# Kernel tuning notes

Hardware: AMD Instinct MI355X
Metric: run time of the kernel (lower is better)

Reference implementation:

```python
import jax, jax.numpy as jnp
import numpy as np

KH, KW, PAD, DIL, STRIDE = 3, 3, 1, 1, 1


def _conv2d(x, w):
    # plain dense conv, NCHW / OIHW, stride 1, pad 1
    return jax.lax.conv_general_dilated(
        x, w, window_strides=(STRIDE, STRIDE),
        padding=[(PAD, PAD), (PAD, PAD)],
        rhs_dilation=(DIL, DIL),
        dimension_numbers=('NCHW', 'OIHW', 'NCHW'))


def _deform_patches(x, offset):
    """Bilinear-sample deformable patches.
    x: [B,C,H,W], offset: [B,2K,Ho,Wo] with per-tap (dy,dx).
    Returns [B,C,K,Ho,Wo]."""
    B, C, H, W = x.shape
    Ho, Wo = offset.shape[2], offset.shape[3]
    K = KH * KW
    off = offset.reshape(B, K, 2, Ho, Wo)

    ky = jnp.repeat(jnp.arange(KH), KW)            # [K]
    kx = jnp.tile(jnp.arange(KW), KH)              # [K]
    base_y = (jnp.arange(Ho) * STRIDE - PAD)[None, :, None] + (DIL * ky)[:, None, None]  # [K,Ho,1]
    base_x = (jnp.arange(Wo) * STRIDE - PAD)[None, None, :] + (DIL * kx)[:, None, None]  # [K,1,Wo]

    sy = base_y[None].astype(x.dtype) + off[:, :, 0]   # [B,K,Ho,Wo]
    sx = base_x[None].astype(x.dtype) + off[:, :, 1]

    y0 = jnp.floor(sy); x0 = jnp.floor(sx)
    ly = sy - y0;       lx = sx - x0
    y0i = y0.astype(jnp.int32); x0i = x0.astype(jnp.int32)

    x_flat = x.reshape(B, C, H * W)

    def corner(yi, xi, wgt):
        valid = (yi >= 0) & (yi < H) & (xi >= 0) & (xi < W)   # zero padding outside
        idx = (jnp.clip(yi, 0, H - 1) * W + jnp.clip(xi, 0, W - 1))  # [B,K,Ho,Wo]
        gath = jax.vmap(lambda img, i: img[:, i.reshape(-1)])(x_flat, idx)  # [B,C,K*Ho*Wo]
        gath = gath.reshape(B, C, K, Ho, Wo)
        return gath * (wgt * valid.astype(x.dtype))[:, None]

    p = corner(y0i,     x0i,     (1 - ly) * (1 - lx))
    p = p + corner(y0i,     x0i + 1, (1 - ly) * lx)
    p = p + corner(y0i + 1, x0i,     ly * (1 - lx))
    p = p + corner(y0i + 1, x0i + 1, ly * lx)
    return p  # [B,C,K,Ho,Wo]


def setup_inputs() -> dict:
    key = jax.random.key(0)
    k1, k2, k3 = jax.random.split(key, 3)
    B, C, H, W = 8, 256, 64, 64
    Cout = 256
    x = jax.random.normal(k1, (B, C, H, W), dtype=jnp.float32)
    offset_w = jax.random.normal(k2, (2 * KH * KW, C, KH, KW), dtype=jnp.float32) * 0.02
    deform_w = jax.random.normal(k3, (Cout, C, KH, KW), dtype=jnp.float32) * 0.02
    return {"x": x, "offset_w": offset_w, "deform_w": deform_w}


def reference(x, offset_w, deform_w):
    # 1) offset-predicting conv
    offset = _conv2d(x, offset_w)                    # [B,2K,H,W]
    # 2) deformable conv = bilinear gather + contraction over (Cin, K)
    patches = _deform_patches(x, offset)             # [B,C,K,H,W]
    Cout = deform_w.shape[0]
    wk = deform_w.reshape(Cout, deform_w.shape[1], KH * KW)
    y = jnp.einsum('bckhw,ock->bohw', patches, wk)   # [B,Cout,H,W]
    # 3) avg + std channel attention (torch.std default: unbiased, ddof=1)
    avg = jnp.mean(y, axis=(2, 3), keepdims=True)
    std = jnp.std(y, axis=(2, 3), keepdims=True, ddof=1)
    attn = jax.nn.sigmoid(avg + std)
    return y * attn
```

## Files before the change

kernel.cpp:

```cpp
#include <hip/hip_runtime.h>
#include <hip/hip_bf16.h>
#include <math.h>

#define C_IN 256
#define H_   64
#define W_   64
#define B_   8
#define COUT 256
#define HW   (H_*W_)

typedef float f32x4 __attribute__((ext_vector_type(4)));
typedef float f32x2 __attribute__((ext_vector_type(2)));
typedef short short8 __attribute__((ext_vector_type(8)));

static __device__ __forceinline__ int pack_bf16x2(float a, float b) {
    __hip_bfloat162 h = __float22bfloat162_rn(make_float2(a, b));
    union { __hip_bfloat162 h; int i; } u; u.h = h;
    return u.i;
}

static __device__ __forceinline__ f32x2 up2(int v) {
    union { int i; float f; } a, b;
    a.i = v << 16;
    b.i = v & 0xffff0000;
    f32x2 r; r[0] = a.f; r[1] = b.f;
    return r;
}

__global__ __launch_bounds__(256) void prep_weights_kernel(
    const float* __restrict__ ow, const float* __restrict__ dw,
    short* __restrict__ wR, short* __restrict__ wO)
{
    int blk = blockIdx.x;
    int k   = blk / 288;
    int row = blk % 288;
    int c   = threadIdx.x;
    int cblk = c >> 6, ks = (c >> 5) & 1, q = (c >> 3) & 3, ce = c & 7;
    union { float f; unsigned u; } a;
    if (row < 256) {
        int o = row;
        a.f = dw[(size_t)o * 2304 + c * 9 + k];
        unsigned r = (a.u + 0x7fffu + ((a.u >> 16) & 1u)) >> 16;
        size_t idx = (size_t)(k * 8 + cblk * 2 + ks) * 8192
                   + (size_t)(o >> 4) * 512 + q * 128 + (o & 15) * 8 + ce;
        wR[idx] = (short)r;
    } else {
        int o = row - 256;
        a.f = (o < 18) ? ow[(size_t)o * 2304 + c * 9 + k] : 0.f;
        unsigned r = (a.u + 0x7fffu + ((a.u >> 16) & 1u)) >> 16;
        size_t idx = (size_t)(k * 8 + cblk * 2 + ks) * 1024
                   + (size_t)(o >> 4) * 512 + q * 128 + (o & 15) * 8 + ce;
        wO[idx] = (short)r;
    }
}

__global__ __launch_bounds__(256) void transpose_x_kernel(
    const float* __restrict__ x, unsigned short* __restrict__ xT)
{
    __shared__ float tile[64][257];
    const int tid = threadIdx.x;
    const int b = blockIdx.x >> 6, h = blockIdx.x & 63;
    const float* xb = x + ((size_t)b << 20) + h * 64;

#pragma unroll
    for (int pass = 0; pass < 16; ++pass) {
        int c  = pass * 16 + (tid >> 4);
        int w0 = (tid & 15) * 4;
        float4 v = *(const float4*)(xb + (size_t)c * 4096 + w0);
        tile[w0][c] = v.x; tile[w0 + 1][c] = v.y;
        tile[w0 + 2][c] = v.z; tile[w0 + 3][c] = v.w;
    }
    __syncthreads();

    int4* ob = (int4*)(xT + ((size_t)blockIdx.x << 14));
#pragma unroll
    for (int pass = 0; pass < 8; ++pass) {
        int idx = pass * 256 + tid;
        int w = idx >> 5, ch8 = idx & 31;
        const float* tr = &tile[w][ch8 * 8];
        int4 pk;
        pk.x = pack_bf16x2(tr[0], tr[1]);
        pk.y = pack_bf16x2(tr[2], tr[3]);
        pk.z = pack_bf16x2(tr[4], tr[5]);
        pk.w = pack_bf16x2(tr[6], tr[7]);
        ob[idx] = pk;
    }
}

__global__ __launch_bounds__(256, 2) void offset_mfma_kernel(
    const unsigned short* __restrict__ xT, const short* __restrict__ wO,
    float* __restrict__ offs)
{
    __shared__ int4 xtile[3 * 66 * 8];

    const int tid = threadIdx.x;
    const int b   = blockIdx.x & 7;
    const int ho  = blockIdx.x >> 3;

    const int wv = tid >> 6;
    const int ln = tid & 63;
    const int lo = ln & 15;
    const int quad = ln >> 4;

    f32x4 acc[2];
    acc[0] = (f32x4){0.f, 0.f, 0.f, 0.f};
    acc[1] = (f32x4){0.f, 0.f, 0.f, 0.f};

    const unsigned short* xbb = xT + ((size_t)b << 20);
    const int4 zero4 = {0, 0, 0, 0};

    const int srow = tid >> 6;
    const int spx  = tid & 63;
    const int syy  = ho + srow - 1;
    const bool svalid = (srow < 3) && (syy >= 0) && (syy < 64);
    const int syc  = min(max(syy, 0), 63);
    const unsigned short* sbase = xbb + (((size_t)(syc * 64 + spx)) << 8);
    const int sslot = spx + 1;

#define OLOAD(CH, G)                                                          \
    if (srow < 3) {                                                           \
        const int4* sp_ = (const int4*)(sbase + (CH));                        \
        _Pragma("unroll")                                                     \
        for (int j = 0; j < 8; ++j) G[j] = sp_[j];                            \
    }
#define OCOMMIT(G)                                                            \
    if (srow < 3) {                                                           \
        _Pragma("unroll")                                                     \
        for (int j = 0; j < 8; ++j)                                           \
            xtile[(srow * 66 + sslot) * 8 + (j ^ (sslot & 7))]                \
                = svalid ? G[j] : zero4;                                      \
    }

    auto mfmaC = [&](int chunk) {
        __builtin_amdgcn_s_setprio(1);
#pragma unroll
        for (int ky = 0; ky < 3; ++ky) {
#pragma unroll
            for (int kx = 0; kx < 3; ++kx) {
#pragma unroll
                for (int ks = 0; ks < 2; ++ks) {
                    int ps = wv * 16 + lo + kx;
                    int cslot = (ks * 4 + quad) ^ (ps & 7);
                    short8 bfr = *(const short8*)&xtile[(ky * 66 + ps) * 8 + cslot];
                    const short* wkb = wO
                        + (size_t)((ky * 3 + kx) * 8 + chunk * 2 + ks) * 1024
                        + ln * 8;
#pragma unroll
                    for (int t = 0; t < 2; ++t) {
                        short8 afr = *(const short8*)(wkb + t * 512);
                        acc[t] = __builtin_amdgcn_mfma_f32_16x16x32_bf16(
                            afr, bfr, acc[t], 0, 0, 0);
                    }
                }
            }
        }
        __builtin_amdgcn_s_setprio(0);
    };

    int4 ga[8], gb[8];
    OLOAD(0, ga);
    OCOMMIT(ga);
    if (srow == 3 && (tid & 63) < 6) {
        int idx = tid & 63;
        int row_ = idx >> 1, s_ = (idx & 1) * 65;
#pragma unroll
        for (int j = 0; j < 8; ++j) xtile[(row_ * 66 + s_) * 8 + j] = zero4;
    }
    __syncthreads();

    OLOAD(64, gb);
    __builtin_amdgcn_sched_barrier(0);
    mfmaC(0);
    __syncthreads();
    OCOMMIT(gb);
    __syncthreads();

    OLOAD(128, ga);
    __builtin_amdgcn_sched_barrier(0);
    mfmaC(1);
    __syncthreads();
    OCOMMIT(ga);
    __syncthreads();

    OLOAD(192, gb);
    __builtin_amdgcn_sched_barrier(0);
    mfmaC(2);
    __syncthreads();
    OCOMMIT(gb);
    __syncthreads();

    mfmaC(3);
#undef OLOAD
#undef OCOMMIT

#pragma unroll
    for (int t = 0; t < 2; ++t) {
#pragma unroll
        for (int r = 0; r < 4; ++r) {
            int o = t * 16 + quad * 4 + r;
            if (o < 18)
                offs[((size_t)b * 18 + o) * HW + ho * 64 + wv * 16 + lo] = acc[t][r];
        }
    }
}

struct afrag { short8 v[2][4]; };

__global__ __launch_bounds__(256, 2) void deform_mfma_kernel(
    const unsigned short* __restrict__ xT, const float* __restrict__ offs,
    const short* __restrict__ wR, float* __restrict__ y,
    float* __restrict__ sum_, float* __restrict__ sumsq_)
{
    __shared__ int4   meta_i[576];
    __shared__ float4 meta_w[576];
    __shared__ int4   bT[2][64 * 8];

    const int tid = threadIdx.x;
    const int b   = blockIdx.x & 7;
    const int ho  = blockIdx.x >> 3;

    for (int e = tid; e < 576; e += 256) {
        int kk  = e >> 6;
        int pxe = e & 63;
        float dy = offs[((size_t)b * 18 + 2 * kk)     * HW + ho * W_ + pxe];
        float dx = offs[((size_t)b * 18 + 2 * kk + 1) * HW + ho * W_ + pxe];
        float sy = (float)(ho - 1 + kk / 3) + dy;
        float sx = (float)(pxe - 1 + kk % 3) + dx;
        float y0f = floorf(sy), x0f = floorf(sx);
        float ly = sy - y0f, lx = sx - x0f;
        int y0 = (int)y0f, x0 = (int)x0f;
        int y1 = y0 + 1, x1 = x0 + 1;
        float wy0 = 1.f - ly, wx0 = 1.f - lx;
        bool vy0 = (y0 >= 0) & (y0 < H_), vy1 = (y1 >= 0) & (y1 < H_);
        bool vx0 = (x0 >= 0) & (x0 < W_), vx1 = (x1 >= 0) & (x1 < W_);
        int cy0 = min(max(y0, 0), H_ - 1), cy1 = min(max(y1, 0), H_ - 1);
        int cx0 = min(max(x0, 0), W_ - 1), cx1 = min(max(x1, 0), W_ - 1);
        int4 ii; float4 ww;
        ii.x = (cy0 * W_ + cx0) << 9;  ww.x = wy0 * wx0 * ((vy0 & vx0) ? 1.f : 0.f);
        ii.y = (cy0 * W_ + cx1) << 9;  ww.y = wy0 * lx  * ((vy0 & vx1) ? 1.f : 0.f);
        ii.z = (cy1 * W_ + cx0) << 9;  ww.z = ly  * wx0 * ((vy1 & vx0) ? 1.f : 0.f);
        ii.w = (cy1 * W_ + cx1) << 9;  ww.w = ly  * lx  * ((vy1 & vx1) ? 1.f : 0.f);
        meta_i[e] = ii;
        meta_w[e] = ww;
    }

    const int px = tid >> 2;
    const int cg = tid & 3;
    const int wv = tid >> 6;
    const int ln = tid & 63;
    const int lo = ln & 15;
    const int quad = ln >> 4;

    f32x4 acc[4][4];
#pragma unroll
    for (int t = 0; t < 4; ++t)
#pragma unroll
        for (int p = 0; p < 4; ++p)
            acc[t][p] = (f32x4){0.f, 0.f, 0.f, 0.f};

    const char* xbb = (const char*)(xT + ((size_t)b << 20) + cg * 16);

#define ISSUE_G(S, G0,G1,G2,G3,G4,G5,G6,G7)                                   \
    {                                                                         \
        int kn_ = (S) >> 2, cn_ = ((S) & 3) << 7;                             \
        int4 ii_ = meta_i[kn_ * 64 + px];                                     \
        const char* xc_ = xbb + cn_;                                          \
        const int4* pA_ = (const int4*)(xc_ + ii_.x);                         \
        const int4* pB_ = (const int4*)(xc_ + ii_.y);                         \
        const int4* pC_ = (const int4*)(xc_ + ii_.z);                         \
        const int4* pD_ = (const int4*)(xc_ + ii_.w);                         \
        G0 = pA_[0]; G1 = pA_[1];                                             \
        G2 = pB_[0]; G3 = pB_[1];                                             \
        G4 = pC_[0]; G5 = pC_[1];                                             \
        G6 = pD_[0]; G7 = pD_[1];                                             \
    }

#define ISSUE_A(S, AF)                                                        \
    {                                                                         \
        const short* wkb_ = wR + (size_t)((((S) >> 2) * 8 + ((S) & 3) * 2))   \
                          * 8192 + wv * 2048 + ln * 8;                        \
        _Pragma("unroll")                                                     \
        for (int ks_ = 0; ks_ < 2; ++ks_)                                     \
            _Pragma("unroll")                                                 \
            for (int t_ = 0; t_ < 4; ++t_)                                    \
                AF.v[ks_][t_] = *(const short8*)(wkb_ + ks_ * 8192 + t_ * 512);\
    }

#define BLEND_W(S, BUF, G0,G1,G2,G3,G4,G5,G6,G7)                              \
    {                                                                         \
        int kn_ = (S) >> 2;                                                   \
        float4 w4_ = meta_w[kn_ * 64 + px];                                   \
        auto bl_ = [&](int av, int bv, int cv, int dv) -> int {               \
            f32x2 r_ = up2(av) * w4_.x + up2(bv) * w4_.y                      \
                     + up2(cv) * w4_.z + up2(dv) * w4_.w;                     \
            return pack_bf16x2(r_[0], r_[1]);                                 \
        };                                                                    \
        int4 o0_, o1_;                                                        \
        o0_.x = bl_(G0.x, G2.x, G4.x, G6.x);                                  \
        o0_.y = bl_(G0.y, G2.y, G4.y, G6.y);                                  \
        o0_.z = bl_(G0.z, G2.z, G4.z, G6.z);                                  \
        o0_.w = bl_(G0.w, G2.w, G4.w, G6.w);                                  \
        o1_.x = bl_(G1.x, G3.x, G5.x, G7.x);                                  \
        o1_.y = bl_(G1.y, G3.y, G5.y, G7.y);                                  \
        o1_.z = bl_(G1.z, G3.z, G5.z, G7.z);                                  \
        o1_.w = bl_(G1.w, G3.w, G5.w, G7.w);                                  \
        bT[BUF][px * 8 + ((2 * cg)     ^ (px & 7))] = o0_;                    \
        bT[BUF][px * 8 + ((2 * cg + 1) ^ (px & 7))] = o1_;                    \
    }

    auto mfmaStage = [&](int buf, const afrag& AF) {
        __builtin_amdgcn_s_setprio(1);
#pragma unroll
        for (int ks = 0; ks < 2; ++ks) {
            int ch = ks * 4 + quad;
            short8 bfr[4];
#pragma unroll
            for (int p = 0; p < 4; ++p) {
                int pp = p * 16 + lo;
                bfr[p] = *(const short8*)&bT[buf][pp * 8 + (ch ^ (pp & 7))];
            }
#pragma unroll
            for (int t = 0; t < 4; ++t)
#pragma unroll
                for (int p = 0; p < 4; ++p)
                    acc[t][p] = __builtin_amdgcn_mfma_f32_16x16x32_bf16(
                        AF.v[ks][t], bfr[p], acc[t][p], 0, 0, 0);
        }
        __builtin_amdgcn_s_setprio(0);
    };

    int4 a0, a1, a2, a3, a4, a5, a6, a7;
    int4 b0, b1, b2, b3, b4, b5, b6, b7;
    afrag afrA, afrB;

    __syncthreads();

    ISSUE_A(0, afrA);
    ISSUE_G(0, a0,a1,a2,a3,a4,a5,a6,a7);
    ISSUE_G(1, b0,b1,b2,b3,b4,b5,b6,b7);
    BLEND_W(0, 0, a0,a1,a2,a3,a4,a5,a6,a7);
    __syncthreads();

#pragma unroll 1
    for (int t = 0; t < 17; ++t) {
        int s = 2 * t;
        ISSUE_A(s + 1, afrB);
        ISSUE_G(s + 2, a0,a1,a2,a3,a4,a5,a6,a7);
        __builtin_amdgcn_sched_barrier(0);
        mfmaStage(0, afrA);
        BLEND_W(s + 1, 1, b0,b1,b2,b3,b4,b5,b6,b7);
        __syncthreads();
        ISSUE_A(s + 2, afrA);
        ISSUE_G(s + 3, b0,b1,b2,b3,b4,b5,b6,b7);
        __builtin_amdgcn_sched_barrier(0);
        mfmaStage(1, afrB);
        BLEND_W(s + 2, 0, a0,a1,a2,a3,a4,a5,a6,a7);
        __syncthreads();
    }
    ISSUE_A(35, afrB);
    __builtin_amdgcn_sched_barrier(0);
    mfmaStage(0, afrA);
    BLEND_W(35, 1, b0,b1,b2,b3,b4,b5,b6,b7);
    __syncthreads();
    mfmaStage(1, afrB);

#undef ISSUE_G
#undef ISSUE_A
#undef BLEND_W

    float* yb = y + ((size_t)b << 20) + ho * 64;
#pragma unroll
    for (int t = 0; t < 4; ++t) {
#pragma unroll
        for (int r = 0; r < 4; ++r) {
            int o = wv * 64 + t * 16 + quad * 4 + r;
            float sv = 0.f, qv = 0.f;
#pragma unroll
            for (int p = 0; p < 4; ++p) {
                float val = acc[t][p][r];
                yb[(size_t)o * HW + p * 16 + lo] = val;
                sv += val;
                qv += val * val;
            }
#pragma unroll
            for (int m = 1; m <= 8; m <<= 1) {
                sv += __shfl_xor(sv, m, 16);
                qv += __shfl_xor(qv, m, 16);
            }
            if (lo == 0) {
                atomicAdd(&sum_[b * COUT + o], sv);
                atomicAdd(&sumsq_[b * COUT + o], qv);
            }
        }
    }
}

__global__ __launch_bounds__(256) void attn_scale_kernel(
    const float* __restrict__ sum_, const float* __restrict__ sumsq_,
    float* __restrict__ y)
{
    int bo = blockIdx.x;
    float s = sum_[bo], q = sumsq_[bo];
    float mean = s * (1.f / 4096.f);
    float var  = (q - s * s * (1.f / 4096.f)) * (1.f / 4095.f);
    float sd   = sqrtf(fmaxf(var, 0.f));
    float attn = 1.f / (1.f + expf(-(mean + sd)));
    float4* yp = (float4*)(y + (size_t)bo * HW);
#pragma unroll
    for (int i = 0; i < 4; ++i) {
        float4 v = yp[threadIdx.x + i * 256];
        v.x *= attn; v.y *= attn; v.z *= attn; v.w *= attn;
        yp[threadIdx.x + i * 256] = v;
    }
}

extern "C" void kernel_launch(void* const* d_in, const int* in_sizes, int n_in,
                              void* d_out, int out_size, void* d_ws, size_t ws_size,
                              hipStream_t stream)
{
    const float* x  = (const float*)d_in[0];
    const float* ow = (const float*)d_in[1];
    const float* dw = (const float*)d_in[2];
    float* out = (float*)d_out;
    float* ws  = (float*)d_ws;

    float*          offs = ws;
    unsigned short* xT   = (unsigned short*)(ws + 589824);
    short*          wR   = (short*)(xT + 8388608);
    short*          wO   = wR + 589824;
    float*          sum_ = (float*)(wO + 73728);
    float*          sumsq_ = sum_ + 2048;

    hipMemsetAsync(sum_, 0, 2 * 2048 * sizeof(float), stream);

    prep_weights_kernel<<<9 * 288, 256, 0, stream>>>(ow, dw, wR, wO);
    transpose_x_kernel<<<512, 256, 0, stream>>>(x, xT);
    offset_mfma_kernel<<<512, 256, 0, stream>>>(xT, wO, offs);
    deform_mfma_kernel<<<512, 256, 0, stream>>>(xT, offs, wR, out, sum_, sumsq_);
    attn_scale_kernel<<<2048, 256, 0, stream>>>(sum_, sumsq_, out);
}
```

Baseline: 199.2 us.

## Process two output rows per deform block with 512 threads and fp16 bilinear weights

The deformable conv kernel now handles two output rows (128 pixels) per block with 512 threads and 8 waves. Each wave computes 32 output channels across 8 pixel tiles instead of 64 channels across 4. Each weight fragment is now reused over twice as many pixels, which halves total weight traffic and the block count. The bilinear corner weights are stored in LDS as packed fp16 to keep LDS use down, at some cost in precision. Register pressure and occupancy shift because of the larger block and the different accumulator shape.

After: 200.2 us. About the same (+0.5%).

```diff
diff --git a/kernel.cpp b/kernel.cpp
--- a/kernel.cpp
+++ b/kernel.cpp
@@ -1,5 +1,6 @@
 #include <hip/hip_runtime.h>
 #include <hip/hip_bf16.h>
+#include <hip/hip_fp16.h>
 #include <math.h>
 
 #define C_IN 256
@@ -24,6 +25,18 @@
     a.i = v << 16;
     b.i = v & 0xffff0000;
     f32x2 r; r[0] = a.f; r[1] = b.f;
+    return r;
+}
+
+static __device__ __forceinline__ unsigned pkhalf2(float a, float b) {
+    __half2 h = __floats2half2_rn(a, b);
+    union { __half2 h; unsigned u; } c; c.h = h;
+    return c.u;
+}
+static __device__ __forceinline__ f32x2 uphalf2(unsigned v) {
+    union { unsigned u; __half2 h; } c; c.u = v;
+    float2 f = __half22float2(c.h);
+    f32x2 r; r[0] = f.x; r[1] = f.y;
     return r;
 }
 
@@ -204,28 +217,31 @@
     }
 }
 
-struct afrag { short8 v[2][4]; };
-
-__global__ __launch_bounds__(256, 2) void deform_mfma_kernel(
+struct afrag2 { short8 v[2][2]; };
+
+__global__ __launch_bounds__(512, 2) void deform_mfma_kernel(
     const unsigned short* __restrict__ xT, const float* __restrict__ offs,
     const short* __restrict__ wR, float* __restrict__ y,
     float* __restrict__ sum_, float* __restrict__ sumsq_)
 {
-    __shared__ int4   meta_i[576];
-    __shared__ float4 meta_w[576];
-    __shared__ int4   bT[2][64 * 8];
+    __shared__ int4  meta_i[1152];
+    __shared__ uint2 meta_w[1152];
+    __shared__ int4  bT[2][128 * 8];
 
     const int tid = threadIdx.x;
     const int b   = blockIdx.x & 7;
-    const int ho  = blockIdx.x >> 3;
-
-    for (int e = tid; e < 576; e += 256) {
-        int kk  = e >> 6;
-        int pxe = e & 63;
-        float dy = offs[((size_t)b * 18 + 2 * kk)     * HW + ho * W_ + pxe];
-        float dx = offs[((size_t)b * 18 + 2 * kk + 1) * HW + ho * W_ + pxe];
-        float sy = (float)(ho - 1 + kk / 3) + dy;
-        float sx = (float)(pxe - 1 + kk % 3) + dx;
+    const int hp  = blockIdx.x >> 3;
+    const int ho0 = hp * 2;
+
+    for (int e = tid; e < 1152; e += 512) {
+        int kk  = e >> 7;
+        int pxe = e & 127;
+        int hoe = ho0 + (pxe >> 6);
+        int xe  = pxe & 63;
+        float dy = offs[((size_t)b * 18 + 2 * kk)     * HW + hoe * W_ + xe];
+        float dx = offs[((size_t)b * 18 + 2 * kk + 1) * HW + hoe * W_ + xe];
+        float sy = (float)(hoe - 1 + kk / 3) + dy;
+        float sx = (float)(xe  - 1 + kk % 3) + dx;
         float y0f = floorf(sy), x0f = floorf(sx);
         float ly = sy - y0f, lx = sx - x0f;
         int y0 = (int)y0f, x0 = (int)x0f;
@@ -235,13 +251,17 @@
         bool vx0 = (x0 >= 0) & (x0 < W_), vx1 = (x1 >= 0) & (x1 < W_);
         int cy0 = min(max(y0, 0), H_ - 1), cy1 = min(max(y1, 0), H_ - 1);
         int cx0 = min(max(x0, 0), W_ - 1), cx1 = min(max(x1, 0), W_ - 1);
-        int4 ii; float4 ww;
-        ii.x = (cy0 * W_ + cx0) << 9;  ww.x = wy0 * wx0 * ((vy0 & vx0) ? 1.f : 0.f);
-        ii.y = (cy0 * W_ + cx1) << 9;  ww.y = wy0 * lx  * ((vy0 & vx1) ? 1.f : 0.f);
-        ii.z = (cy1 * W_ + cx0) << 9;  ww.z = ly  * wx0 * ((vy1 & vx0) ? 1.f : 0.f);
-        ii.w = (cy1 * W_ + cx1) << 9;  ww.w = ly  * lx  * ((vy1 & vx1) ? 1.f : 0.f);
+        int4 ii;
+        float wA = wy0 * wx0 * ((vy0 & vx0) ? 1.f : 0.f);
+        float wB = wy0 * lx  * ((vy0 & vx1) ? 1.f : 0.f);
+        float wC = ly  * wx0 * ((vy1 & vx0) ? 1.f : 0.f);
+        float wD = ly  * lx  * ((vy1 & vx1) ? 1.f : 0.f);
+        ii.x = (cy0 * W_ + cx0) << 9;
+        ii.y = (cy0 * W_ + cx1) << 9;
+        ii.z = (cy1 * W_ + cx0) << 9;
+        ii.w = (cy1 * W_ + cx1) << 9;
         meta_i[e] = ii;
-        meta_w[e] = ww;
+        meta_w[e] = make_uint2(pkhalf2(wA, wB), pkhalf2(wC, wD));
     }
 
     const int px = tid >> 2;
@@ -251,11 +271,11 @@
     const int lo = ln & 15;
     const int quad = ln >> 4;
 
-    f32x4 acc[4][4];
-#pragma unroll
-    for (int t = 0; t < 4; ++t)
-#pragma unroll
-        for (int p = 0; p < 4; ++p)
+    f32x4 acc[2][8];
+#pragma unroll
+    for (int t = 0; t < 2; ++t)
+#pragma unroll
+        for (int p = 0; p < 8; ++p)
             acc[t][p] = (f32x4){0.f, 0.f, 0.f, 0.f};
 
     const char* xbb = (const char*)(xT + ((size_t)b << 20) + cg * 16);
@@ -263,7 +283,7 @@
 #define ISSUE_G(S, G0,G1,G2,G3,G4,G5,G6,G7)                                   \
     {                                                                         \
         int kn_ = (S) >> 2, cn_ = ((S) & 3) << 7;                             \
-        int4 ii_ = meta_i[kn_ * 64 + px];                                     \
+        int4 ii_ = meta_i[kn_ * 128 + px];                                    \
         const char* xc_ = xbb + cn_;                                          \
         const int4* pA_ = (const int4*)(xc_ + ii_.x);                         \
         const int4* pB_ = (const int4*)(xc_ + ii_.y);                         \
@@ -278,21 +298,23 @@
 #define ISSUE_A(S, AF)                                                        \
     {                                                                         \
         const short* wkb_ = wR + (size_t)((((S) >> 2) * 8 + ((S) & 3) * 2))   \
-                          * 8192 + wv * 2048 + ln * 8;                        \
+                          * 8192 + wv * 1024 + ln * 8;                        \
         _Pragma("unroll")                                                     \
         for (int ks_ = 0; ks_ < 2; ++ks_)                                     \
             _Pragma("unroll")                                                 \
-            for (int t_ = 0; t_ < 4; ++t_)                                    \
+            for (int t_ = 0; t_ < 2; ++t_)                                    \
                 AF.v[ks_][t_] = *(const short8*)(wkb_ + ks_ * 8192 + t_ * 512);\
     }
 
 #define BLEND_W(S, BUF, G0,G1,G2,G3,G4,G5,G6,G7)                              \
     {                                                                         \
         int kn_ = (S) >> 2;                                                   \
-        float4 w4_ = meta_w[kn_ * 64 + px];                                   \
+        uint2 wp_ = meta_w[kn_ * 128 + px];                                   \
+        f32x2 wab_ = uphalf2(wp_.x);                                          \
+        f32x2 wcd_ = uphalf2(wp_.y);                                          \
         auto bl_ = [&](int av, int bv, int cv, int dv) -> int {               \
-            f32x2 r_ = up2(av) * w4_.x + up2(bv) * w4_.y                      \
-                     + up2(cv) * w4_.z + up2(dv) * w4_.w;                     \
+            f32x2 r_ = up2(av) * wab_[0] + up2(bv) * wab_[1]                  \
+                     + up2(cv) * wcd_[0] + up2(dv) * wcd_[1];                 \
             return pack_bf16x2(r_[0], r_[1]);                                 \
         };                                                                    \
         int4 o0_, o1_;                                                        \
@@ -308,21 +330,21 @@
         bT[BUF][px * 8 + ((2 * cg + 1) ^ (px & 7))] = o1_;                    \
     }
 
-    auto mfmaStage = [&](int buf, const afrag& AF) {
+    auto mfmaStage = [&](int buf, const afrag2& AF) {
         __builtin_amdgcn_s_setprio(1);
 #pragma unroll
         for (int ks = 0; ks < 2; ++ks) {
             int ch = ks * 4 + quad;
-            short8 bfr[4];
-#pragma unroll
-            for (int p = 0; p < 4; ++p) {
+            short8 bfr[8];
+#pragma unroll
+            for (int p = 0; p < 8; ++p) {
                 int pp = p * 16 + lo;
                 bfr[p] = *(const short8*)&bT[buf][pp * 8 + (ch ^ (pp & 7))];
             }
 #pragma unroll
-            for (int t = 0; t < 4; ++t)
-#pragma unroll
-                for (int p = 0; p < 4; ++p)
+            for (int t = 0; t < 2; ++t)
+#pragma unroll
+                for (int p = 0; p < 8; ++p)
                     acc[t][p] = __builtin_amdgcn_mfma_f32_16x16x32_bf16(
                         AF.v[ks][t], bfr[p], acc[t][p], 0, 0, 0);
         }
@@ -331,7 +353,7 @@
 
     int4 a0, a1, a2, a3, a4, a5, a6, a7;
     int4 b0, b1, b2, b3, b4, b5, b6, b7;
-    afrag afrA, afrB;
+    afrag2 afrA, afrB;
 
     __syncthreads();
 
@@ -368,17 +390,17 @@
 #undef ISSUE_A
 #undef BLEND_W
 
-    float* yb = y + ((size_t)b << 20) + ho * 64;
-#pragma unroll
-    for (int t = 0; t < 4; ++t) {
+    float* yb = y + ((size_t)b << 20);
+#pragma unroll
+    for (int t = 0; t < 2; ++t) {
 #pragma unroll
         for (int r = 0; r < 4; ++r) {
-            int o = wv * 64 + t * 16 + quad * 4 + r;
+            int o = wv * 32 + t * 16 + quad * 4 + r;
             float sv = 0.f, qv = 0.f;
 #pragma unroll
-            for (int p = 0; p < 4; ++p) {
+            for (int p = 0; p < 8; ++p) {
                 float val = acc[t][p][r];
-                yb[(size_t)o * HW + p * 16 + lo] = val;
+                yb[((size_t)o << 12) + (ho0 + (p >> 2)) * 64 + (p & 3) * 16 + lo] = val;
                 sv += val;
                 qv += val * val;
             }
@@ -436,6 +458,6 @@
     prep_weights_kernel<<<9 * 288, 256, 0, stream>>>(ow, dw, wR, wO);
     transpose_x_kernel<<<512, 256, 0, stream>>>(x, xT);
     offset_mfma_kernel<<<512, 256, 0, stream>>>(xT, wO, offs);
-    deform_mfma_kernel<<<512, 256, 0, stream>>>(xT, offs, wR, out, sum_, sumsq_);
+    deform_mfma_kernel<<<256, 512, 0, stream>>>(xT, offs, wR, out, sum_, sumsq_);
     attn_scale_kernel<<<2048, 256, 0, stream>>>(sum_, sumsq_, out);
 }
```

## Warp-specialize deform conv into producer gather waves and consumer MFMA waves

Applied to the files above, without the earlier changes.

The deformable conv kernel now launches 512 threads. Four producer waves do the bilinear gather, blend and LDS stores, and four consumer waves load weights and run the MFMAs. The LDS ring grows from 2 to 4 buffers and the syncs become a custom barrier that only waits on LDS counters. The aim is to overlap gather latency with matrix work across separate waves. The cost is more registers per block, which may cap occupancy at the requested 2 blocks, plus barrier coordination between roles.

New measurement: 222.9 us. +11.9%, slower.

```diff
diff --git a/kernel.cpp b/kernel.cpp
--- a/kernel.cpp
+++ b/kernel.cpp
@@ -25,6 +25,12 @@
     b.i = v & 0xffff0000;
     f32x2 r; r[0] = a.f; r[1] = b.f;
     return r;
+}
+
+static __device__ __forceinline__ void wg_barrier_lds() {
+    asm volatile("s_waitcnt lgkmcnt(0)" ::: "memory");
+    __builtin_amdgcn_s_barrier();
+    __builtin_amdgcn_sched_barrier(0);
 }
 
 __global__ __launch_bounds__(256) void prep_weights_kernel(
@@ -206,20 +212,20 @@
 
 struct afrag { short8 v[2][4]; };
 
-__global__ __launch_bounds__(256, 2) void deform_mfma_kernel(
+__global__ __launch_bounds__(512, 2) void deform_mfma_kernel(
     const unsigned short* __restrict__ xT, const float* __restrict__ offs,
     const short* __restrict__ wR, float* __restrict__ y,
     float* __restrict__ sum_, float* __restrict__ sumsq_)
 {
     __shared__ int4   meta_i[576];
     __shared__ float4 meta_w[576];
-    __shared__ int4   bT[2][64 * 8];
+    __shared__ int4   bT[4][64 * 8];
 
     const int tid = threadIdx.x;
     const int b   = blockIdx.x & 7;
     const int ho  = blockIdx.x >> 3;
 
-    for (int e = tid; e < 576; e += 256) {
+    for (int e = tid; e < 576; e += 512) {
         int kk  = e >> 6;
         int pxe = e & 63;
         float dy = offs[((size_t)b * 18 + 2 * kk)     * HW + ho * W_ + pxe];
@@ -244,11 +250,15 @@
         meta_w[e] = ww;
     }
 
+    const int wave  = tid >> 6;
+    const bool isP  = wave < 4;
+
     const int px = tid >> 2;
     const int cg = tid & 3;
-    const int wv = tid >> 6;
-    const int ln = tid & 63;
-    const int lo = ln & 15;
+
+    const int wv2  = wave - 4;
+    const int ln   = tid & 63;
+    const int lo   = ln & 15;
     const int quad = ln >> 4;
 
     f32x4 acc[4][4];
@@ -278,7 +288,7 @@
 #define ISSUE_A(S, AF)                                                        \
     {                                                                         \
         const short* wkb_ = wR + (size_t)((((S) >> 2) * 8 + ((S) & 3) * 2))   \
-                          * 8192 + wv * 2048 + ln * 8;                        \
+                          * 8192 + wv2 * 2048 + ln * 8;                       \
         _Pragma("unroll")                                                     \
         for (int ks_ = 0; ks_ < 2; ++ks_)                                     \
             _Pragma("unroll")                                                 \
@@ -286,7 +296,7 @@
                 AF.v[ks_][t_] = *(const short8*)(wkb_ + ks_ * 8192 + t_ * 512);\
     }
 
-#define BLEND_W(S, BUF, G0,G1,G2,G3,G4,G5,G6,G7)                              \
+#define BLEND_W(S, G0,G1,G2,G3,G4,G5,G6,G7)                                   \
     {                                                                         \
         int kn_ = (S) >> 2;                                                   \
         float4 w4_ = meta_w[kn_ * 64 + px];                                   \
@@ -304,11 +314,12 @@
         o1_.y = bl_(G1.y, G3.y, G5.y, G7.y);                                  \
         o1_.z = bl_(G1.z, G3.z, G5.z, G7.z);                                  \
         o1_.w = bl_(G1.w, G3.w, G5.w, G7.w);                                  \
-        bT[BUF][px * 8 + ((2 * cg)     ^ (px & 7))] = o0_;                    \
-        bT[BUF][px * 8 + ((2 * cg + 1) ^ (px & 7))] = o1_;                    \
-    }
-
-    auto mfmaStage = [&](int buf, const afrag& AF) {
+        bT[(S) & 3][px * 8 + ((2 * cg)     ^ (px & 7))] = o0_;                \
+        bT[(S) & 3][px * 8 + ((2 * cg + 1) ^ (px & 7))] = o1_;                \
+    }
+
+    auto mfmaStage = [&](int s, const afrag& AF) {
+        const int buf = s & 3;
         __builtin_amdgcn_s_setprio(1);
 #pragma unroll
         for (int ks = 0; ks < 2; ++ks) {
@@ -335,61 +346,77 @@
 
     __syncthreads();
 
-    ISSUE_A(0, afrA);
-    ISSUE_G(0, a0,a1,a2,a3,a4,a5,a6,a7);
-    ISSUE_G(1, b0,b1,b2,b3,b4,b5,b6,b7);
-    BLEND_W(0, 0, a0,a1,a2,a3,a4,a5,a6,a7);
-    __syncthreads();
+    if (isP) {
+        ISSUE_G(0, a0,a1,a2,a3,a4,a5,a6,a7);
+        ISSUE_G(1, b0,b1,b2,b3,b4,b5,b6,b7);
+        BLEND_W(0, a0,a1,a2,a3,a4,a5,a6,a7);
+    } else {
+        ISSUE_A(0, afrA);
+    }
+    wg_barrier_lds();
 
 #pragma unroll 1
     for (int t = 0; t < 17; ++t) {
         int s = 2 * t;
-        ISSUE_A(s + 1, afrB);
-        ISSUE_G(s + 2, a0,a1,a2,a3,a4,a5,a6,a7);
+        if (isP) {
+            ISSUE_G(s + 2, a0,a1,a2,a3,a4,a5,a6,a7);
+            __builtin_amdgcn_sched_barrier(0);
+            BLEND_W(s + 1, b0,b1,b2,b3,b4,b5,b6,b7);
+        } else {
+            ISSUE_A(s + 1, afrB);
+            __builtin_amdgcn_sched_barrier(0);
+            mfmaStage(s, afrA);
+        }
+        wg_barrier_lds();
+        if (isP) {
+            ISSUE_G(s + 3, b0,b1,b2,b3,b4,b5,b6,b7);
+            __builtin_amdgcn_sched_barrier(0);
+            BLEND_W(s + 2, a0,a1,a2,a3,a4,a5,a6,a7);
+        } else {
+            ISSUE_A(s + 2, afrA);
+            __builtin_amdgcn_sched_barrier(0);
+            mfmaStage(s + 1, afrB);
+        }
+        wg_barrier_lds();
+    }
+    if (isP) {
+        BLEND_W(35, b0,b1,b2,b3,b4,b5,b6,b7);
+    } else {
+        ISSUE_A(35, afrB);
         __builtin_amdgcn_sched_barrier(0);
-        mfmaStage(0, afrA);
-        BLEND_W(s + 1, 1, b0,b1,b2,b3,b4,b5,b6,b7);
-        __syncthreads();
-        ISSUE_A(s + 2, afrA);
-        ISSUE_G(s + 3, b0,b1,b2,b3,b4,b5,b6,b7);
-        __builtin_amdgcn_sched_barrier(0);
-        mfmaStage(1, afrB);
-        BLEND_W(s + 2, 0, a0,a1,a2,a3,a4,a5,a6,a7);
-        __syncthreads();
-    }
-    ISSUE_A(35, afrB);
-    __builtin_amdgcn_sched_barrier(0);
-    mfmaStage(0, afrA);
-    BLEND_W(35, 1, b0,b1,b2,b3,b4,b5,b6,b7);
-    __syncthreads();
-    mfmaStage(1, afrB);
+        mfmaStage(34, afrA);
+    }
+    wg_barrier_lds();
+    if (!isP) mfmaStage(35, afrB);
 
 #undef ISSUE_G
 #undef ISSUE_A
 #undef BLEND_W
 
-    float* yb = y + ((size_t)b << 20) + ho * 64;
-#pragma unroll
-    for (int t = 0; t < 4; ++t) {
-#pragma unroll
-        for (int r = 0; r < 4; ++r) {
-            int o = wv * 64 + t * 16 + quad * 4 + r;
-            float sv = 0.f, qv = 0.f;
-#pragma unroll
-            for (int p = 0; p < 4; ++p) {
-                float val = acc[t][p][r];
-                yb[(size_t)o * HW + p * 16 + lo] = val;
-                sv += val;
-                qv += val * val;
-            }
-#pragma unroll
-            for (int m = 1; m <= 8; m <<= 1) {
-                sv += __shfl_xor(sv, m, 16);
-                qv += __shfl_xor(qv, m, 16);
-            }
-            if (lo == 0) {
-                atomicAdd(&sum_[b * COUT + o], sv);
-                atomicAdd(&sumsq_[b * COUT + o], qv);
+    if (!isP) {
+        float* yb = y + ((size_t)b << 20) + ho * 64;
+#pragma unroll
+        for (int t = 0; t < 4; ++t) {
+#pragma unroll
+            for (int r = 0; r < 4; ++r) {
+                int o = wv2 * 64 + t * 16 + quad * 4 + r;
+                float sv = 0.f, qv = 0.f;
+#pragma unroll
+                for (int p = 0; p < 4; ++p) {
+                    float val = acc[t][p][r];
+                    yb[(size_t)o * HW + p * 16 + lo] = val;
+                    sv += val;
+                    qv += val * val;
+                }
+#pragma unroll
+                for (int m = 1; m <= 8; m <<= 1) {
+                    sv += __shfl_xor(sv, m, 16);
+                    qv += __shfl_xor(qv, m, 16);
+                }
+                if (lo == 0) {
+                    atomicAdd(&sum_[b * COUT + o], sv);
+                    atomicAdd(&sumsq_[b * COUT + o], qv);
+                }
             }
         }
     }
@@ -436,6 +463,6 @@
     prep_weights_kernel<<<9 * 288, 256, 0, stream>>>(ow, dw, wR, wO);
     transpose_x_kernel<<<512, 256, 0, stream>>>(x, xT);
     offset_mfma_kernel<<<512, 256, 0, stream>>>(xT, wO, offs);
-    deform_mfma_kernel<<<512, 256, 0, stream>>>(xT, offs, wR, out, sum_, sumsq_);
+    deform_mfma_kernel<<<512, 512, 0, stream>>>(xT, offs, wR, out, sum_, sumsq_);
     attn_scale_kernel<<<2048, 256, 0, stream>>>(sum_, sumsq_, out);
 }
```
